# Kernel tuning notes

Hardware: AMD Instinct MI355X
Metric: run time of the kernel (lower is better)

## Reference

```python
import jax, jax.numpy as jnp
import numpy as np

T, B, OBS, A, P, NB, H = 32, 256, 1024, 16, 600, 601, 128


def setup_inputs() -> dict:
    key = jax.random.key(0)
    ks = jax.random.split(key, 32)
    f32 = jnp.float32

    def rn(k, shape, scale):
        return jax.random.normal(k, shape, dtype=f32) * scale

    hh = 1.0 / np.sqrt(H)
    inp = {
        "obs_seq": rn(ks[0], (T, B, OBS), 1.0),
        # backbone MLP (512, 512)
        "bb_w1": rn(ks[1], (OBS, 512), 1.0 / np.sqrt(OBS)), "bb_b1": jnp.zeros((512,), f32),
        "bb_w2": rn(ks[2], (512, 512), 1.0 / np.sqrt(512)), "bb_b2": jnp.zeros((512,), f32),
        # feedforward heads (final layers init std=0.01, bias 0 per module)
        "pol_w": rn(ks[3], (512, A), 0.01), "pol_b": jnp.zeros((A,), f32),
        "y_w": rn(ks[4], (512, P), 0.01), "y_b": jnp.zeros((P,), f32),
        "ci_w": rn(ks[5], (512, H), 1.0 / np.sqrt(512)), "ci_b": jnp.zeros((H,), f32),
        # LSTMCell(A, 128): gate order i,f,g,o as in torch
        "w_ih": rn(ks[6], (A, 4 * H), hh), "w_hh": rn(ks[7], (H, 4 * H), hh),
        "b_ih": rn(ks[8], (4 * H,), hh), "b_hh": rn(ks[9], (4 * H,), hh),
        # z / q / aux_pi MLPs: Linear(128,128) -> ReLU -> Linear(128, out)
        "z_w1": rn(ks[10], (H, H), hh), "z_b1": jnp.zeros((H,), f32),
        "z_w2": rn(ks[11], (H, P), 0.01), "z_b2": jnp.zeros((P,), f32),
        "q_w1": rn(ks[12], (H, H), hh), "q_b1": jnp.zeros((H,), f32),
        "q_w2": rn(ks[13], (H, NB), 0.01), "q_b2": jnp.zeros((NB,), f32),
        "a_w1": rn(ks[14], (H, H), hh), "a_b1": jnp.zeros((H,), f32),
        "a_w2": rn(ks[15], (H, A), 0.01), "a_b2": jnp.zeros((A,), f32),
    }
    return inp


def reference(obs_seq, bb_w1, bb_b1, bb_w2, bb_b2, pol_w, pol_b, y_w, y_b,
              ci_w, ci_b, w_ih, w_hh, b_ih, b_hh,
              z_w1, z_b1, z_w2, z_b2, q_w1, q_b1, q_w2, q_b2,
              a_w1, a_b1, a_w2, a_b2):
    Tn, Bn = obs_seq.shape[:2]
    x = obs_seq.reshape(Tn * Bn, -1)  # feedforward across time: fold T into batch
    emb = jax.nn.relu(jax.nn.relu(x @ bb_w1 + bb_b1) @ bb_w2 + bb_b2)  # [N,512]
    logits = emb @ pol_w + pol_b  # [N,A]
    y = emb @ y_w + y_b           # [N,P]
    c0 = emb @ ci_w + ci_b        # [N,H]
    h0 = jnp.tanh(c0)

    # one_hot(a) @ W_ih^T == row a of W_ih (input-to-gate contribution per action)
    in_gates = w_ih + b_ih  # [A, 4H]

    def step(carry, ig):
        h, c = carry
        g = ig + h @ w_hh + b_hh  # [N,4H]
        i, f, gg, o = jnp.split(g, 4, axis=-1)  # torch gate order i,f,g,o
        c = jax.nn.sigmoid(f) * c + jax.nn.sigmoid(i) * jnp.tanh(gg)
        h = jax.nn.sigmoid(o) * jnp.tanh(c)
        return (h, c), h

    _, h_all = jax.lax.scan(step, (h0, c0), in_gates)  # [A, N, H]

    def mlp(hx, w1, b1, w2, b2):
        return jax.nn.relu(hx @ w1 + b1) @ w2 + b2

    def to_tba(arr):
        Aa, N, D = arr.shape
        return arr.reshape(Aa, Tn, Bn, D).transpose(1, 2, 0, 3)  # [T,B,A,D]

    z = to_tba(mlp(h_all, z_w1, z_b1, z_w2, z_b2))
    q = to_tba(mlp(h_all, q_w1, q_b1, q_w2, q_b2))
    aux_pi = to_tba(mlp(h_all, a_w1, a_b1, a_w2, a_b2))
    return (logits.reshape(Tn, Bn, -1), y.reshape(Tn, Bn, -1), z, q, aux_pi)
```

## Files before the change

kernel.cpp:

```cpp
#include <hip/hip_runtime.h>
#include <stdint.h>

typedef short bf16x8 __attribute__((ext_vector_type(8)));
typedef float f32x4 __attribute__((ext_vector_type(4)));
typedef unsigned short u16x4 __attribute__((ext_vector_type(4)));

__device__ __forceinline__ unsigned short f2b(float f) {
  union { float f; unsigned u; } v; v.f = f;
  unsigned r = v.u + 0x7fffu + ((v.u >> 16) & 1u);
  return (unsigned short)(r >> 16);
}
__device__ __forceinline__ float fsigm(float x) { return 1.f / (1.f + __expf(-x)); }
__device__ __forceinline__ float ftanh(float x) {
  float t = __expf(-2.f * fabsf(x));
  float r = (1.f - t) / (1.f + t);
  return copysignf(r, x);
}

struct TD { const float* in; unsigned short* out; int R, C; };
struct TDs { TD d[12]; };

__global__ __launch_bounds__(256) void tconv_all(TDs ds) {
  TD t = ds.d[blockIdx.z];
  int c0 = blockIdx.x * 32, r0 = blockIdx.y * 32;
  if (c0 >= t.C || r0 >= t.R) return;
  __shared__ float tl[32][33];
  int tx = threadIdx.x & 31, ty = threadIdx.x >> 5;
  #pragma unroll
  for (int i = 0; i < 32; i += 8) {
    int r = r0 + ty + i, c = c0 + tx;
    tl[ty + i][tx] = (r < t.R && c < t.C) ? t.in[(size_t)r * t.C + c] : 0.f;
  }
  __syncthreads();
  #pragma unroll
  for (int i = 0; i < 32; i += 8) {
    int c = c0 + ty + i, r = r0 + tx;
    if (c < t.C && r < t.R) t.out[(size_t)c * t.R + r] = f2b(tl[tx][ty + i]);
  }
}

__global__ __launch_bounds__(256) void conv_k(const float* __restrict__ in,
                                              unsigned short* __restrict__ out, int n) {
  int i = (blockIdx.x * 256 + threadIdx.x) * 8;
  if (i >= n) return;
  float4 a = *(const float4*)(in + i);
  float4 b = *(const float4*)(in + i + 4);
  bf16x8 v;
  v[0] = (short)f2b(a.x); v[1] = (short)f2b(a.y); v[2] = (short)f2b(a.z); v[3] = (short)f2b(a.w);
  v[4] = (short)f2b(b.x); v[5] = (short)f2b(b.y); v[6] = (short)f2b(b.z); v[7] = (short)f2b(b.w);
  *(bf16x8*)(out + i) = v;
}

template <int ACT, bool OBF16>
__global__ __launch_bounds__(256) void gemm_k(const unsigned short* __restrict__ A,
                                              const unsigned short* __restrict__ BT,
                                              const float* __restrict__ bias,
                                              void* __restrict__ Cp,
                                              int M, int N, int K, int ldC) {
  __shared__ unsigned short As[64][40];
  __shared__ unsigned short Bs[64][40];
  const int tid = threadIdx.x;
  const int n0 = blockIdx.x * 64;
  const int m0 = blockIdx.y * 64;
  const int wid = tid >> 6, lane = tid & 63;
  const int wm = (wid >> 1) * 32, wn = (wid & 1) * 32;
  const int lr = lane & 15, lk = lane >> 4;
  const int sr = tid >> 2, sc = (tid & 3) * 8;

  f32x4 acc[2][2] = {};

  for (int k0 = 0; k0 < K; k0 += 32) {
    *(bf16x8*)&As[sr][sc] = *(const bf16x8*)(A + (size_t)(m0 + sr) * K + k0 + sc);
    {
      int n = n0 + sr;
      bf16x8 v = {};
      if (n < N) v = *(const bf16x8*)(BT + (size_t)n * K + k0 + sc);
      *(bf16x8*)&Bs[sr][sc] = v;
    }
    __syncthreads();
    bf16x8 af[2], bfr[2];
    #pragma unroll
    for (int mi = 0; mi < 2; mi++) af[mi] = *(const bf16x8*)&As[wm + mi * 16 + lr][lk * 8];
    #pragma unroll
    for (int ni = 0; ni < 2; ni++) bfr[ni] = *(const bf16x8*)&Bs[wn + ni * 16 + lr][lk * 8];
    #pragma unroll
    for (int mi = 0; mi < 2; mi++)
      #pragma unroll
      for (int ni = 0; ni < 2; ni++)
        acc[mi][ni] = __builtin_amdgcn_mfma_f32_16x16x32_bf16(af[mi], bfr[ni], acc[mi][ni], 0, 0, 0);
    __syncthreads();
  }

  #pragma unroll
  for (int mi = 0; mi < 2; mi++)
    #pragma unroll
    for (int ni = 0; ni < 2; ni++) {
      int col = n0 + wn + ni * 16 + lr;
      if (col >= N) continue;
      float bv = bias[col];
      #pragma unroll
      for (int r = 0; r < 4; r++) {
        int row = m0 + wm + mi * 16 + lk * 4 + r;
        float v = acc[mi][ni][r] + bv;
        if (ACT == 1) v = fmaxf(v, 0.f);
        if (OBF16) ((unsigned short*)Cp)[(size_t)row * ldC + col] = f2b(v);
        else       ((float*)Cp)[(size_t)row * ldC + col] = v;
      }
    }
}

__global__ __launch_bounds__(1024) void lstm_k(const float* __restrict__ c0,
                                               const unsigned short* __restrict__ whhT,
                                               const float* __restrict__ w_ih,
                                               const float* __restrict__ b_ih,
                                               const float* __restrict__ b_hh,
                                               unsigned short* __restrict__ h_all) {
  __shared__ float G[32][516];
  __shared__ float cst[32][128];
  __shared__ unsigned short hst[32][136];
  const int tid = threadIdx.x, lane = tid & 63, wid = tid >> 6;
  const int r0 = blockIdx.x * 32;
  const int lr = lane & 15, lk = lane >> 4;

  bf16x8 wv[2][4];
  #pragma unroll
  for (int nj = 0; nj < 2; nj++)
    #pragma unroll
    for (int ks = 0; ks < 4; ks++)
      wv[nj][ks] = *(const bf16x8*)(whhT + (size_t)(wid * 32 + nj * 16 + lr) * 128 + ks * 32 + lk * 8);

  const int j = tid & 127;
  const int rb = tid >> 7;
  const float bs0 = b_ih[j]       + b_hh[j];
  const float bs1 = b_ih[j + 128] + b_hh[j + 128];
  const float bs2 = b_ih[j + 256] + b_hh[j + 256];
  const float bs3 = b_ih[j + 384] + b_hh[j + 384];

  {
    int r = tid >> 5, j4 = (tid & 31) * 4;
    float4 c4 = *(const float4*)(c0 + (size_t)(r0 + r) * 128 + j4);
    *(f32x4*)&cst[r][j4] = f32x4{c4.x, c4.y, c4.z, c4.w};
    u16x4 h4;
    h4[0] = f2b(ftanh(c4.x)); h4[1] = f2b(ftanh(c4.y));
    h4[2] = f2b(ftanh(c4.z)); h4[3] = f2b(ftanh(c4.w));
    *(u16x4*)&hst[r][j4] = h4;
  }
  __syncthreads();

  for (int a = 0; a < 16; a++) {
    f32x4 acc[2][2] = {};
    #pragma unroll
    for (int ks = 0; ks < 4; ks++) {
      bf16x8 af0 = *(const bf16x8*)&hst[lr][ks * 32 + lk * 8];
      bf16x8 af1 = *(const bf16x8*)&hst[16 + lr][ks * 32 + lk * 8];
      #pragma unroll
      for (int nj = 0; nj < 2; nj++) {
        acc[0][nj] = __builtin_amdgcn_mfma_f32_16x16x32_bf16(af0, wv[nj][ks], acc[0][nj], 0, 0, 0);
        acc[1][nj] = __builtin_amdgcn_mfma_f32_16x16x32_bf16(af1, wv[nj][ks], acc[1][nj], 0, 0, 0);
      }
    }
    #pragma unroll
    for (int mi = 0; mi < 2; mi++)
      #pragma unroll
      for (int nj = 0; nj < 2; nj++)
        #pragma unroll
        for (int rr = 0; rr < 4; rr++)
          G[mi * 16 + lk * 4 + rr][wid * 32 + nj * 16 + lr] = acc[mi][nj][rr];
    __syncthreads();

    const float* ig = w_ih + a * 512;
    const float ig0 = ig[j], ig1 = ig[j + 128], ig2 = ig[j + 256], ig3 = ig[j + 384];
    #pragma unroll
    for (int it = 0; it < 4; it++) {
      int r = rb + it * 8;
      float gi = G[r][j]       + ig0 + bs0;
      float gf = G[r][j + 128] + ig1 + bs1;
      float gg = G[r][j + 256] + ig2 + bs2;
      float go = G[r][j + 384] + ig3 + bs3;
      float c = cst[r][j];
      float cn = fsigm(gf) * c + fsigm(gi) * ftanh(gg);
      float h = fsigm(go) * ftanh(cn);
      cst[r][j] = cn;
      unsigned short hb = f2b(h);
      hst[r][j] = hb;
      h_all[((size_t)(r0 + r) * 16 + a) * 128 + j] = hb;
    }
    __syncthreads();
  }
}

__global__ __launch_bounds__(64) void heads_k(
    const unsigned short* __restrict__ hall,
    const unsigned short* __restrict__ w1cat,
    const unsigned short* __restrict__ w2cat,
    const float* __restrict__ zb1, const float* __restrict__ qb1, const float* __restrict__ ab1,
    const float* __restrict__ zb2, const float* __restrict__ qb2, const float* __restrict__ ab2,
    float* __restrict__ oz, float* __restrict__ oq, float* __restrict__ oa) {
  __shared__ unsigned short hp[32][136];
  const int lane = threadIdx.x & 63;
  const int lr = lane & 15, lk = lane >> 4;
  const int r0 = blockIdx.x * 32;

  bf16x8 av[2][4];
  #pragma unroll
  for (int jf = 0; jf < 2; jf++)
    #pragma unroll
    for (int ks = 0; ks < 4; ks++)
      av[jf][ks] = *(const bf16x8*)(hall + (size_t)(r0 + jf * 16 + lr) * 128 + ks * 32 + lk * 8);

  const float* B1a[3] = {zb1, qb1, ab1};
  const float* B2a[3] = {zb2, qb2, ab2};
  float*       OOa[3] = {oz, oq, oa};

  #pragma unroll
  for (int hi = 0; hi < 3; hi++) {
    const int Nh = (hi == 0) ? 600 : (hi == 1) ? 601 : 16;
    const int so = (hi == 0) ? 0 : (hi == 1) ? 600 : 1201;
    const int NF = (hi == 2) ? 1 : 38;
    const float* b1 = B1a[hi];
    const float* b2 = B2a[hi];
    float* Oh = OOa[hi];

    #pragma unroll
    for (int nf = 0; nf < 8; nf++) {
      bf16x8 w1v[4];
      #pragma unroll
      for (int ks = 0; ks < 4; ks++)
        w1v[ks] = *(const bf16x8*)(w1cat + (size_t)(hi * 128 + nf * 16 + lr) * 128 + ks * 32 + lk * 8);
      f32x4 hacc[2] = {};
      #pragma unroll
      for (int ks = 0; ks < 4; ks++)
        #pragma unroll
        for (int jf = 0; jf < 2; jf++)
          hacc[jf] = __builtin_amdgcn_mfma_f32_16x16x32_bf16(w1v[ks], av[jf][ks], hacc[jf], 0, 0, 0);
      f32x4 bb = *(const f32x4*)(b1 + nf * 16 + lk * 4);
      #pragma unroll
      for (int jf = 0; jf < 2; jf++) {
        u16x4 h4;
        #pragma unroll
        for (int rr = 0; rr < 4; rr++)
          h4[rr] = f2b(fmaxf(hacc[jf][rr] + bb[rr], 0.f));
        *(u16x4*)&hp[jf * 16 + lr][nf * 16 + lk * 4] = h4;
      }
    }
    asm volatile("s_waitcnt lgkmcnt(0)" ::: "memory");
    __builtin_amdgcn_sched_barrier(0);

    bf16x8 hv[2][4];
    #pragma unroll
    for (int jf = 0; jf < 2; jf++)
      #pragma unroll
      for (int ks = 0; ks < 4; ks++)
        hv[jf][ks] = *(const bf16x8*)&hp[jf * 16 + lr][ks * 32 + lk * 8];

    for (int f0 = 0; f0 < NF; f0 += 10) {
      f32x4 oacc[10][2];
      #pragma unroll
      for (int ff = 0; ff < 10; ff++) {
        int f = f0 + ff;
        if (f < NF) {
          int wrow = f * 16 + lr; if (wrow > Nh - 1) wrow = Nh - 1;
          bf16x8 w2v[4];
          #pragma unroll
          for (int ks = 0; ks < 4; ks++)
            w2v[ks] = *(const bf16x8*)(w2cat + (size_t)(so + wrow) * 128 + ks * 32 + lk * 8);
          oacc[ff][0] = f32x4{0.f, 0.f, 0.f, 0.f};
          oacc[ff][1] = f32x4{0.f, 0.f, 0.f, 0.f};
          #pragma unroll
          for (int ks = 0; ks < 4; ks++)
            #pragma unroll
            for (int jf = 0; jf < 2; jf++)
              oacc[ff][jf] = __builtin_amdgcn_mfma_f32_16x16x32_bf16(w2v[ks], hv[jf][ks], oacc[ff][jf], 0, 0, 0);
          int bc = f * 16 + lk * 4;
          f32x4 bb;
          if (bc + 3 < Nh) {
            bb = *(const f32x4*)(b2 + bc);
          } else {
            #pragma unroll
            for (int rr = 0; rr < 4; rr++) bb[rr] = (bc + rr < Nh) ? b2[bc + rr] : 0.f;
          }
          oacc[ff][0] += bb;
          oacc[ff][1] += bb;
        }
      }
      #pragma unroll
      for (int ff = 0; ff < 10; ff++) {
        int f = f0 + ff;
        if (f < NF) {
          int col = f * 16 + lk * 4;
          #pragma unroll
          for (int jf = 0; jf < 2; jf++) {
            float* p = Oh + (size_t)(r0 + jf * 16 + lr) * Nh + col;
            if (col + 3 < Nh) {
              f32x4 v = oacc[ff][jf];
              __builtin_memcpy(p, &v, 16);
            } else {
              #pragma unroll
              for (int rr = 0; rr < 4; rr++)
                if (col + rr < Nh) p[rr] = oacc[ff][jf][rr];
            }
          }
        }
      }
    }
  }
}

extern "C" void kernel_launch(void* const* d_in, const int* in_sizes, int n_in,
                              void* d_out, int out_size, void* d_ws, size_t ws_size,
                              hipStream_t stream) {
  const float* obs   = (const float*)d_in[0];
  const float* bb_w1 = (const float*)d_in[1];
  const float* bb_b1 = (const float*)d_in[2];
  const float* bb_w2 = (const float*)d_in[3];
  const float* bb_b2 = (const float*)d_in[4];
  const float* pol_w = (const float*)d_in[5];
  const float* pol_b = (const float*)d_in[6];
  const float* y_w   = (const float*)d_in[7];
  const float* y_b   = (const float*)d_in[8];
  const float* ci_w  = (const float*)d_in[9];
  const float* ci_b  = (const float*)d_in[10];
  const float* w_ih  = (const float*)d_in[11];
  const float* w_hh  = (const float*)d_in[12];
  const float* b_ih  = (const float*)d_in[13];
  const float* b_hh  = (const float*)d_in[14];
  const float* z_w1  = (const float*)d_in[15];
  const float* z_b1  = (const float*)d_in[16];
  const float* z_w2  = (const float*)d_in[17];
  const float* z_b2  = (const float*)d_in[18];
  const float* q_w1  = (const float*)d_in[19];
  const float* q_b1  = (const float*)d_in[20];
  const float* q_w2  = (const float*)d_in[21];
  const float* q_b2  = (const float*)d_in[22];
  const float* a_w1  = (const float*)d_in[23];
  const float* a_b1  = (const float*)d_in[24];
  const float* a_w2  = (const float*)d_in[25];
  const float* a_b2  = (const float*)d_in[26];

  float* out = (float*)d_out;
  float* out_logits = out;
  float* out_y      = out + 131072;
  float* out_z      = out + 5046272;
  float* out_q      = out + 83689472;
  float* out_a      = out + 162463744;

  uint8_t* ws = (uint8_t*)d_ws;
  size_t off = 0;
  auto alc = [&](size_t bytes) -> void* {
    void* p = ws + off;
    off = (off + bytes + 255) & ~(size_t)255;
    return p;
  };
  unsigned short* W1T  = (unsigned short*)alc((size_t)512 * 1024 * 2);
  unsigned short* W2T  = (unsigned short*)alc((size_t)512 * 512 * 2);
  unsigned short* polT = (unsigned short*)alc((size_t)16 * 512 * 2);
  unsigned short* yT   = (unsigned short*)alc((size_t)600 * 512 * 2);
  unsigned short* ciT  = (unsigned short*)alc((size_t)128 * 512 * 2);
  unsigned short* whhT = (unsigned short*)alc((size_t)512 * 128 * 2);
  unsigned short* zw1T = (unsigned short*)alc((size_t)128 * 128 * 2);
  unsigned short* qw1T = (unsigned short*)alc((size_t)128 * 128 * 2);
  unsigned short* aw1T = (unsigned short*)alc((size_t)128 * 128 * 2);
  unsigned short* zw2T = (unsigned short*)alc((size_t)600 * 128 * 2);
  unsigned short* qw2T = (unsigned short*)alc((size_t)601 * 128 * 2);
  unsigned short* aw2T = (unsigned short*)alc((size_t)16 * 128 * 2);
  unsigned short* obsb = (unsigned short*)alc((size_t)8192 * 1024 * 2);
  unsigned short* hid1 = (unsigned short*)alc((size_t)8192 * 512 * 2);
  unsigned short* emb  = (unsigned short*)alc((size_t)8192 * 512 * 2);
  float*          c0b  = (float*)alc((size_t)8192 * 128 * 4);
  unsigned short* hall = (unsigned short*)alc((size_t)8192 * 16 * 128 * 2);
  (void)ws_size; (void)in_sizes; (void)n_in; (void)out_size;

  dim3 B256(256);

  TDs td;
  td.d[0]  = {bb_w1, W1T, 1024, 512};
  td.d[1]  = {bb_w2, W2T, 512, 512};
  td.d[2]  = {pol_w, polT, 512, 16};
  td.d[3]  = {y_w,   yT,   512, 600};
  td.d[4]  = {ci_w,  ciT,  512, 128};
  td.d[5]  = {w_hh,  whhT, 128, 512};
  td.d[6]  = {z_w1,  zw1T, 128, 128};
  td.d[7]  = {z_w2,  zw2T, 128, 600};
  td.d[8]  = {q_w1,  qw1T, 128, 128};
  td.d[9]  = {q_w2,  qw2T, 128, 601};
  td.d[10] = {a_w1,  aw1T, 128, 128};
  td.d[11] = {a_w2,  aw2T, 128, 16};
  tconv_all<<<dim3(19, 32, 12), B256, 0, stream>>>(td);

  conv_k<<<dim3(4096), B256, 0, stream>>>(obs, obsb, 8192 * 1024);

  gemm_k<1, true><<<dim3(8, 128), B256, 0, stream>>>(obsb, W1T, bb_b1, hid1, 8192, 512, 1024, 512);
  gemm_k<1, true><<<dim3(8, 128), B256, 0, stream>>>(hid1, W2T, bb_b2, emb,  8192, 512, 512,  512);
  gemm_k<0, false><<<dim3(1, 128),  B256, 0, stream>>>(emb, polT, pol_b, out_logits, 8192, 16,  512, 16);
  gemm_k<0, false><<<dim3(10, 128), B256, 0, stream>>>(emb, yT,   y_b,   out_y,      8192, 600, 512, 600);
  gemm_k<0, false><<<dim3(2, 128),  B256, 0, stream>>>(emb, ciT,  ci_b,  c0b,        8192, 128, 512, 128);
  lstm_k<<<dim3(256), dim3(1024), 0, stream>>>(c0b, whhT, w_ih, b_ih, b_hh, hall);
  heads_k<<<dim3(4096), dim3(64), 0, stream>>>(hall,
                                               zw1T, zw2T,
                                               z_b1, q_b1, a_b1,
                                               z_b2, q_b2, a_b2,
                                               out_z, out_q, out_a);
}
```

Baseline: 502.7 us.

## Restructure heads kernel to 4-wave blocks with LDS-staged coalesced output stores

```diff
diff --git a/kernel.cpp b/kernel.cpp
--- a/kernel.cpp
+++ b/kernel.cpp
@@ -189,24 +189,23 @@
   }
 }
 
-__global__ __launch_bounds__(64) void heads_k(
+__global__ __launch_bounds__(256) void heads_k(
     const unsigned short* __restrict__ hall,
     const unsigned short* __restrict__ w1cat,
     const unsigned short* __restrict__ w2cat,
     const float* __restrict__ zb1, const float* __restrict__ qb1, const float* __restrict__ ab1,
     const float* __restrict__ zb2, const float* __restrict__ qb2, const float* __restrict__ ab2,
     float* __restrict__ oz, float* __restrict__ oq, float* __restrict__ oa) {
-  __shared__ unsigned short hp[32][136];
-  const int lane = threadIdx.x & 63;
+  __shared__ unsigned short hp[16][136];
+  __shared__ float ot[16][612];
+  const int tid = threadIdx.x, lane = tid & 63, wid = tid >> 6;
   const int lr = lane & 15, lk = lane >> 4;
-  const int r0 = blockIdx.x * 32;
-
-  bf16x8 av[2][4];
-  #pragma unroll
-  for (int jf = 0; jf < 2; jf++)
-    #pragma unroll
-    for (int ks = 0; ks < 4; ks++)
-      av[jf][ks] = *(const bf16x8*)(hall + (size_t)(r0 + jf * 16 + lr) * 128 + ks * 32 + lk * 8);
+  const int r0 = blockIdx.x * 16;
+
+  bf16x8 av[4];
+  #pragma unroll
+  for (int ks = 0; ks < 4; ks++)
+    av[ks] = *(const bf16x8*)(hall + (size_t)(r0 + lr) * 128 + ks * 32 + lk * 8);
 
   const float* B1a[3] = {zb1, qb1, ab1};
   const float* B2a[3] = {zb2, qb2, ab2};
@@ -222,87 +221,69 @@
     float* Oh = OOa[hi];
 
     #pragma unroll
-    for (int nf = 0; nf < 8; nf++) {
+    for (int jj = 0; jj < 2; jj++) {
+      int nf = wid * 2 + jj;
       bf16x8 w1v[4];
       #pragma unroll
       for (int ks = 0; ks < 4; ks++)
         w1v[ks] = *(const bf16x8*)(w1cat + (size_t)(hi * 128 + nf * 16 + lr) * 128 + ks * 32 + lk * 8);
-      f32x4 hacc[2] = {};
+      f32x4 hacc = {};
       #pragma unroll
       for (int ks = 0; ks < 4; ks++)
-        #pragma unroll
-        for (int jf = 0; jf < 2; jf++)
-          hacc[jf] = __builtin_amdgcn_mfma_f32_16x16x32_bf16(w1v[ks], av[jf][ks], hacc[jf], 0, 0, 0);
+        hacc = __builtin_amdgcn_mfma_f32_16x16x32_bf16(w1v[ks], av[ks], hacc, 0, 0, 0);
       f32x4 bb = *(const f32x4*)(b1 + nf * 16 + lk * 4);
-      #pragma unroll
-      for (int jf = 0; jf < 2; jf++) {
-        u16x4 h4;
-        #pragma unroll
-        for (int rr = 0; rr < 4; rr++)
-          h4[rr] = f2b(fmaxf(hacc[jf][rr] + bb[rr], 0.f));
-        *(u16x4*)&hp[jf * 16 + lr][nf * 16 + lk * 4] = h4;
+      u16x4 h4;
+      #pragma unroll
+      for (int rr = 0; rr < 4; rr++)
+        h4[rr] = f2b(fmaxf(hacc[rr] + bb[rr], 0.f));
+      *(u16x4*)&hp[lr][nf * 16 + lk * 4] = h4;
+    }
+    __syncthreads();
+
+    bf16x8 hv[4];
+    #pragma unroll
+    for (int ks = 0; ks < 4; ks++)
+      hv[ks] = *(const bf16x8*)&hp[lr][ks * 32 + lk * 8];
+
+    for (int f = wid; f < NF; f += 4) {
+      int wrow = f * 16 + lr; if (wrow > Nh - 1) wrow = Nh - 1;
+      bf16x8 w2v[4];
+      #pragma unroll
+      for (int ks = 0; ks < 4; ks++)
+        w2v[ks] = *(const bf16x8*)(w2cat + (size_t)(so + wrow) * 128 + ks * 32 + lk * 8);
+      f32x4 oacc = {};
+      #pragma unroll
+      for (int ks = 0; ks < 4; ks++)
+        oacc = __builtin_amdgcn_mfma_f32_16x16x32_bf16(w2v[ks], hv[ks], oacc, 0, 0, 0);
+      int bc = f * 16 + lk * 4;
+      f32x4 bb;
+      #pragma unroll
+      for (int rr = 0; rr < 4; rr++) bb[rr] = (bc + rr < Nh) ? b2[bc + rr] : 0.f;
+      *(f32x4*)&ot[lr][f * 16 + lk * 4] = oacc + bb;
+    }
+    __syncthreads();
+
+    if (hi == 2) {
+      if (tid < 64) {
+        int r = tid >> 2, c = (tid & 3) * 4;
+        f32x4 v = *(const f32x4*)&ot[r][c];
+        *(f32x4*)(Oh + (size_t)(r0 + r) * 16 + c) = v;
       }
-    }
-    asm volatile("s_waitcnt lgkmcnt(0)" ::: "memory");
-    __builtin_amdgcn_sched_barrier(0);
-
-    bf16x8 hv[2][4];
-    #pragma unroll
-    for (int jf = 0; jf < 2; jf++)
-      #pragma unroll
-      for (int ks = 0; ks < 4; ks++)
-        hv[jf][ks] = *(const bf16x8*)&hp[jf * 16 + lr][ks * 32 + lk * 8];
-
-    for (int f0 = 0; f0 < NF; f0 += 10) {
-      f32x4 oacc[10][2];
-      #pragma unroll
-      for (int ff = 0; ff < 10; ff++) {
-        int f = f0 + ff;
-        if (f < NF) {
-          int wrow = f * 16 + lr; if (wrow > Nh - 1) wrow = Nh - 1;
-          bf16x8 w2v[4];
-          #pragma unroll
-          for (int ks = 0; ks < 4; ks++)
-            w2v[ks] = *(const bf16x8*)(w2cat + (size_t)(so + wrow) * 128 + ks * 32 + lk * 8);
-          oacc[ff][0] = f32x4{0.f, 0.f, 0.f, 0.f};
-          oacc[ff][1] = f32x4{0.f, 0.f, 0.f, 0.f};
-          #pragma unroll
-          for (int ks = 0; ks < 4; ks++)
-            #pragma unroll
-            for (int jf = 0; jf < 2; jf++)
-              oacc[ff][jf] = __builtin_amdgcn_mfma_f32_16x16x32_bf16(w2v[ks], hv[jf][ks], oacc[ff][jf], 0, 0, 0);
-          int bc = f * 16 + lk * 4;
-          f32x4 bb;
-          if (bc + 3 < Nh) {
-            bb = *(const f32x4*)(b2 + bc);
-          } else {
-            #pragma unroll
-            for (int rr = 0; rr < 4; rr++) bb[rr] = (bc + rr < Nh) ? b2[bc + rr] : 0.f;
-          }
-          oacc[ff][0] += bb;
-          oacc[ff][1] += bb;
+    } else {
+      int c = tid * 4;
+      #pragma unroll
+      for (int r = 0; r < 16; r++) {
+        if (c < 600) {
+          f32x4 v = *(const f32x4*)&ot[r][c];
+          float* p = Oh + (size_t)(r0 + r) * Nh + c;
+          if (Nh == 600) *(f32x4*)p = v;
+          else __builtin_memcpy(p, &v, 16);
+        } else if (c == 600 && Nh == 601) {
+          Oh[(size_t)(r0 + r) * Nh + 600] = ot[r][600];
         }
       }
-      #pragma unroll
-      for (int ff = 0; ff < 10; ff++) {
-        int f = f0 + ff;
-        if (f < NF) {
-          int col = f * 16 + lk * 4;
-          #pragma unroll
-          for (int jf = 0; jf < 2; jf++) {
-            float* p = Oh + (size_t)(r0 + jf * 16 + lr) * Nh + col;
-            if (col + 3 < Nh) {
-              f32x4 v = oacc[ff][jf];
-              __builtin_memcpy(p, &v, 16);
-            } else {
-              #pragma unroll
-              for (int rr = 0; rr < 4; rr++)
-                if (col + rr < Nh) p[rr] = oacc[ff][jf][rr];
-            }
-          }
-        }
-      }
-    }
+    }
+    __syncthreads();
   }
 }
 
@@ -395,9 +376,9 @@
   gemm_k<0, false><<<dim3(10, 128), B256, 0, stream>>>(emb, yT,   y_b,   out_y,      8192, 600, 512, 600);
   gemm_k<0, false><<<dim3(2, 128),  B256, 0, stream>>>(emb, ciT,  ci_b,  c0b,        8192, 128, 512, 128);
   lstm_k<<<dim3(256), dim3(1024), 0, stream>>>(c0b, whhT, w_ih, b_ih, b_hh, hall);
-  heads_k<<<dim3(4096), dim3(64), 0, stream>>>(hall,
-                                               zw1T, zw2T,
-                                               z_b1, q_b1, a_b1,
-                                               z_b2, q_b2, a_b2,
-                                               out_z, out_q, out_a);
-}
+  heads_k<<<dim3(8192), B256, 0, stream>>>(hall,
+                                           zw1T, zw2T,
+                                           z_b1, q_b1, a_b1,
+                                           z_b2, q_b2, a_b2,
+                                           out_z, out_q, out_a);
+}
```

Measured after the change: 599.0 us. +19.2%, slower.
